# Kernel tuning notes

Hardware: AMD Instinct MI355X
Metric: run time of the kernel (lower is better)

## Reference

```python
import jax, jax.numpy as jnp
import numpy as np

E, TOPK = 8, 2
N_EMBD, TEXT_DIM, FULL = 1024, 1024, 1024
BS, SEQ = 8, 512

def setup_inputs() -> dict:
    key = jax.random.key(0)
    ks = jax.random.split(key, 8)
    return {
        "x": jax.random.normal(ks[0], (BS, SEQ, N_EMBD), jnp.float32),
        "dec_embeddings": jax.random.normal(ks[1], (BS, TEXT_DIM), jnp.float32),
        # router is zero-init in the module, but use small random weights so top-k is non-degenerate
        "router_w": jax.random.normal(ks[2], (E, TEXT_DIM), jnp.float32) * 0.02,
        "router_b": jnp.zeros((E,), jnp.float32),
        "w1": jax.random.normal(ks[3], (E, N_EMBD, N_EMBD), jnp.float32) * 0.02,
        "w2": jax.random.normal(ks[4], (E, N_EMBD, FULL), jnp.float32) * 0.02,
        "b1": jnp.zeros((E, 1, N_EMBD), jnp.float32),
        "b2": jnp.zeros((E, 1, FULL), jnp.float32),
    }

def reference(x, dec_embeddings, router_w, router_b, w1, w2, b1, b2):
    bs, seqlen, n_embd = x.shape
    logits = dec_embeddings @ router_w.T + router_b          # (bs, E)
    gate_probs = jax.nn.softmax(logits, axis=-1)
    topk_w, topk_idx = jax.lax.top_k(gate_probs, TOPK)       # (bs, k)
    topk_w = topk_w / jnp.sum(topk_w, axis=-1, keepdims=True)
    # dense all-expert 2-layer MLP (as written in the original)
    hidden = jax.nn.relu(jnp.einsum('bsn,enh->ebsh', x, w1) + b1[:, None])   # (E,bs,S,H)
    out_all = jnp.einsum('ebsh,ehf->ebsf', hidden, w2) + b2[:, None]          # (E,bs,S,F)
    out_b = jnp.transpose(out_all, (1, 0, 2, 3))             # (bs,E,S,F)
    # gather top-k expert outputs per batch item and combine
    sel = jnp.take_along_axis(out_b, topk_idx[:, :, None, None], axis=1)      # (bs,k,S,F)
    final_output = jnp.sum(topk_w[:, :, None, None] * sel, axis=1)            # (bs,S,F)
    combined_mask = jnp.max(jax.nn.one_hot(topk_idx, E, dtype=x.dtype), axis=1)  # (bs,E)
    aux_loss = E * jnp.sum(jnp.mean(gate_probs, axis=0) * jnp.mean(combined_mask, axis=0))
    return final_output, aux_loss, combined_mask, logits
```

## Files before the change

### kernel.cpp

```cpp
#include <hip/hip_runtime.h>
#include <hip/hip_bf16.h>
#include <stdint.h>

#define EXP 8
#define DIM 1024
#define SEQL 512
#define BATCH 8
#define OUT_FINAL_N (BATCH * SEQL * DIM)
#define OFF_AUX    4194304
#define OFF_MASK   4194305
#define OFF_LOGITS 4194369

typedef __bf16 bf16_t;
typedef bf16_t bf16x8 __attribute__((ext_vector_type(8)));
typedef bf16_t bf16x4 __attribute__((ext_vector_type(4)));
typedef float  f32x4  __attribute__((ext_vector_type(4)));

typedef __attribute__((address_space(1))) void* as1p;
typedef __attribute__((address_space(3))) void* as3p;

__device__ __forceinline__ void glds16(const void* g, void* l) {
  __builtin_amdgcn_global_load_lds((as1p)(void*)g, (as3p)l, 16, 0, 0);
}

__global__ __launch_bounds__(256) void prep_kernel(
    const float* __restrict__ x, const float* __restrict__ dec,
    const float* __restrict__ rw, const float* __restrict__ rb,
    const float* __restrict__ w1, const float* __restrict__ w2,
    bf16_t* __restrict__ xb, bf16_t* __restrict__ w1t, bf16_t* __restrict__ w2t,
    float* __restrict__ out_aux, float* __restrict__ out_mask,
    float* __restrict__ out_logits, int* __restrict__ idx_ws,
    float* __restrict__ w_ws) {
  __shared__ float tile[64][65];
  __shared__ float part[256];
  __shared__ float lg64[64];
  __shared__ float probs[64];
  __shared__ float msk[64];
  const int bid = blockIdx.x;
  const int t = threadIdx.x;

  if (bid < 4096) {
    const int z = bid >> 8;
    const int rem = bid & 255;
    const int r0 = (rem >> 4) * 64, c0 = (rem & 15) * 64;
    const float* src = (z < 8) ? (w1 + (size_t)z * DIM * DIM)
                               : (w2 + (size_t)(z - 8) * DIM * DIM);
    bf16_t* dst = (z < 8) ? (w1t + (size_t)z * DIM * DIM)
                          : (w2t + (size_t)(z - 8) * DIM * DIM);
    const int rr = t >> 4, cc = t & 15;
#pragma unroll
    for (int i = 0; i < 4; ++i) {
      const int row = rr + i * 16;
      const float4 v = *(const float4*)(src + (size_t)(r0 + row) * DIM + c0 + cc * 4);
      tile[row][cc * 4 + 0] = v.x;
      tile[row][cc * 4 + 1] = v.y;
      tile[row][cc * 4 + 2] = v.z;
      tile[row][cc * 4 + 3] = v.w;
    }
    __syncthreads();
#pragma unroll
    for (int i = 0; i < 4; ++i) {
      const int dc = rr + i * 16;
      bf16x4 o;
      o[0] = (bf16_t)tile[cc * 4 + 0][dc];
      o[1] = (bf16_t)tile[cc * 4 + 1][dc];
      o[2] = (bf16_t)tile[cc * 4 + 2][dc];
      o[3] = (bf16_t)tile[cc * 4 + 3][dc];
      *(bf16x4*)(dst + (size_t)(c0 + dc) * DIM + r0 + cc * 4) = o;
    }
  } else if (bid < 4096 + 1024) {
    const int i0 = (bid - 4096) * 1024 + t;
#pragma unroll
    for (int i = 0; i < 4; ++i) {
      float4 v = ((const float4*)x)[i0 + i * 256];
      bf16x4 o;
      o[0] = (bf16_t)v.x; o[1] = (bf16_t)v.y; o[2] = (bf16_t)v.z; o[3] = (bf16_t)v.w;
      ((bf16x4*)xb)[i0 + i * 256] = o;
    }
  } else {
    const int p = t >> 2, seg = t & 3;
    const int b = p >> 3, e = p & 7;
    const float4* dv = (const float4*)(dec + b * DIM + seg * 256);
    const float4* wv = (const float4*)(rw + e * DIM + seg * 256);
    float s = 0.f;
#pragma unroll 8
    for (int i = 0; i < 64; ++i) {
      float4 a = dv[i], c = wv[i];
      s += a.x * c.x + a.y * c.y + a.z * c.z + a.w * c.w;
    }
    part[t] = s;
    __syncthreads();
    if (seg == 0) {
      float l = part[t] + part[t + 1] + part[t + 2] + part[t + 3] + rb[e];
      lg64[p] = l;
      out_logits[p] = l;
    }
    __syncthreads();
    if (t < 8) {
      float l[8];
      float mx = -1e30f;
#pragma unroll
      for (int k = 0; k < 8; ++k) { l[k] = lg64[t * 8 + k]; mx = fmaxf(mx, l[k]); }
      float pe[8];
      float sum = 0.f;
#pragma unroll
      for (int k = 0; k < 8; ++k) { pe[k] = expf(l[k] - mx); sum += pe[k]; }
      float inv = 1.f / sum;
#pragma unroll
      for (int k = 0; k < 8; ++k) { pe[k] *= inv; probs[t * 8 + k] = pe[k]; }
      int i0 = 0;
#pragma unroll
      for (int k = 1; k < 8; ++k) if (pe[k] > pe[i0]) i0 = k;
      int i1 = (i0 == 0) ? 1 : 0;
#pragma unroll
      for (int k = 0; k < 8; ++k) if (k != i0 && pe[k] > pe[i1]) i1 = k;
      float p0 = pe[i0], p1 = pe[i1];
      float invs = 1.f / (p0 + p1);
      idx_ws[t * 2] = i0;
      idx_ws[t * 2 + 1] = i1;
      w_ws[t * 2] = p0 * invs;
      w_ws[t * 2 + 1] = p1 * invs;
#pragma unroll
      for (int k = 0; k < 8; ++k) {
        float m = (k == i0 || k == i1) ? 1.f : 0.f;
        msk[t * 8 + k] = m;
        out_mask[t * 8 + k] = m;
      }
    }
    __syncthreads();
    if (t == 0) {
      float aux = 0.f;
#pragma unroll
      for (int k = 0; k < 8; ++k) {
        float mp = 0.f, mm = 0.f;
#pragma unroll
        for (int bb = 0; bb < 8; ++bb) { mp += probs[bb * 8 + k]; mm += msk[bb * 8 + k]; }
        aux += (mp * 0.125f) * (mm * 0.125f);
      }
      out_aux[0] = 8.f * aux;
    }
  }
}

__device__ __forceinline__ void gemm_kloop(const bf16_t* __restrict__ A,
                                           const bf16_t* __restrict__ Bt,
                                           char* sA, char* sB,
                                           int tid, f32x4 acc[4][4]) {
  const int lane = tid & 63;
  const int w = tid >> 6;
  const int wr = w >> 1, wc = w & 1;
  const int m15 = lane & 15, q = lane >> 4;

  const int rl = tid >> 2;
  const int cp = (tid & 3) ^ (rl & 3);
  const bf16_t* ga0 = A + (size_t)rl * DIM + cp * 8;
  const bf16_t* ga1 = ga0 + (size_t)64 * DIM;
  const bf16_t* gb0 = Bt + (size_t)rl * DIM + cp * 8;
  const bf16_t* gb1 = gb0 + (size_t)64 * DIM;
  char* la0 = sA + tid * 16;
  char* la1 = sA + 4096 + tid * 16;
  char* lb0 = sB + tid * 16;
  char* lb1 = sB + 4096 + tid * 16;

  const char* ra[4];
  const char* rb[4];
#pragma unroll
  for (int i = 0; i < 4; ++i) {
    int r = wr * 64 + i * 16 + m15;
    ra[i] = sA + r * 64 + ((q ^ (r & 3)) * 16);
    int n = wc * 64 + i * 16 + m15;
    rb[i] = sB + n * 64 + ((q ^ (n & 3)) * 16);
  }

  for (int kt = 0; kt < DIM; kt += 32) {
    glds16(ga0 + kt, la0);
    glds16(ga1 + kt, la1);
    glds16(gb0 + kt, lb0);
    glds16(gb1 + kt, lb1);
    __syncthreads();
    bf16x8 af[4], bfr[4];
#pragma unroll
    for (int i = 0; i < 4; ++i) af[i] = *(const bf16x8*)ra[i];
#pragma unroll
    for (int j = 0; j < 4; ++j) bfr[j] = *(const bf16x8*)rb[j];
#pragma unroll
    for (int i = 0; i < 4; ++i)
#pragma unroll
      for (int j = 0; j < 4; ++j)
        acc[i][j] = __builtin_amdgcn_mfma_f32_16x16x32_bf16(af[i], bfr[j], acc[i][j], 0, 0, 0);
    __syncthreads();
  }
}

__global__ __launch_bounds__(256) void gemm1_kernel(const bf16_t* __restrict__ xb,
                                                    const bf16_t* __restrict__ w1t,
                                                    const float* __restrict__ b1,
                                                    const int* __restrict__ topk_idx,
                                                    bf16_t* __restrict__ hidden) {
  __shared__ __align__(16) char smem[16384];
  const int tid = threadIdx.x;
  const int bN = blockIdx.x, bM = blockIdx.y, slot = blockIdx.z;
  const int b = slot >> 1;
  const int e = topk_idx[slot];

  const bf16_t* A = xb + ((size_t)b * SEQL + bM * 128) * DIM;
  const bf16_t* Bt = w1t + ((size_t)e * DIM + bN * 128) * DIM;

  f32x4 acc[4][4];
#pragma unroll
  for (int i = 0; i < 4; ++i)
#pragma unroll
    for (int j = 0; j < 4; ++j) acc[i][j] = {0.f, 0.f, 0.f, 0.f};

  gemm_kloop(A, Bt, smem, smem + 8192, tid, acc);

  const int lane = tid & 63, w = tid >> 6;
  const int wr = w >> 1, wc = w & 1;
  const int m15 = lane & 15, q = lane >> 4;
  const float* be = b1 + e * DIM;
  bf16_t* H = hidden + (size_t)slot * SEQL * DIM;
#pragma unroll
  for (int i = 0; i < 4; ++i) {
    int row = bM * 128 + wr * 64 + i * 16 + q * 4;
#pragma unroll
    for (int j = 0; j < 4; ++j) {
      int col = bN * 128 + wc * 64 + j * 16 + m15;
      float bias = be[col];
#pragma unroll
      for (int r = 0; r < 4; ++r) {
        float v = acc[i][j][r] + bias;
        H[(size_t)(row + r) * DIM + col] = (bf16_t)fmaxf(v, 0.f);
      }
    }
  }
}

__global__ __launch_bounds__(512) void gemm2_kernel(const bf16_t* __restrict__ hidden,
                                                    const bf16_t* __restrict__ w2t,
                                                    const float* __restrict__ b2,
                                                    const int* __restrict__ topk_idx,
                                                    const float* __restrict__ topk_w,
                                                    float* __restrict__ out) {
  __shared__ __align__(16) char smem[32768];
  const int tid = threadIdx.x;
  const int g = tid >> 8;
  const int t = tid & 255;
  const int bN = blockIdx.x, bM = blockIdx.y, b = blockIdx.z;
  const int e = topk_idx[b * 2 + g];
  const float sg = topk_w[b * 2 + g];

  char* sA = smem + g * 16384;
  char* sB = smem + g * 16384 + 8192;

  f32x4 acc[4][4];
#pragma unroll
  for (int i = 0; i < 4; ++i)
#pragma unroll
    for (int j = 0; j < 4; ++j) acc[i][j] = {0.f, 0.f, 0.f, 0.f};

  const bf16_t* A = hidden + ((size_t)(b * 2 + g) * SEQL + bM * 128) * DIM;
  const bf16_t* Bt = w2t + ((size_t)e * DIM + bN * 128) * DIM;
  gemm_kloop(A, Bt, sA, sB, t, acc);

  float* scr = (float*)smem;
  const int lane = t & 63, wv = t >> 6;
  const int wr = wv >> 1, wc = wv & 1;
  const int m15 = lane & 15, q = lane >> 4;
  const float w0 = topk_w[b * 2], w1v = topk_w[b * 2 + 1];
  const float* be0 = b2 + topk_idx[b * 2] * DIM;
  const float* be1 = b2 + topk_idx[b * 2 + 1] * DIM;
  float* O = out + (size_t)b * SEQL * DIM;

#pragma unroll
  for (int half = 0; half < 2; ++half) {
    __syncthreads();
    if (g == 1) {
#pragma unroll
      for (int ii = 0; ii < 2; ++ii)
#pragma unroll
        for (int j = 0; j < 4; ++j)
#pragma unroll
          for (int r = 0; r < 4; ++r)
            scr[(ii * 16 + j * 4 + r) * 256 + t] = sg * acc[half * 2 + ii][j][r];
    }
    __syncthreads();
    if (g == 0) {
#pragma unroll
      for (int ii = 0; ii < 2; ++ii) {
        const int i = half * 2 + ii;
        const int row = bM * 128 + wr * 64 + i * 16 + q * 4;
#pragma unroll
        for (int j = 0; j < 4; ++j) {
          const int col = bN * 128 + wc * 64 + j * 16 + m15;
          const float bb = w0 * be0[col] + w1v * be1[col];
#pragma unroll
          for (int r = 0; r < 4; ++r) {
            O[(size_t)(row + r) * DIM + col] =
                sg * acc[i][j][r] + scr[(ii * 16 + j * 4 + r) * 256 + t] + bb;
          }
        }
      }
    }
  }
}

extern "C" void kernel_launch(void* const* d_in, const int* in_sizes, int n_in,
                              void* d_out, int out_size, void* d_ws, size_t ws_size,
                              hipStream_t stream) {
  const float* x   = (const float*)d_in[0];
  const float* dec = (const float*)d_in[1];
  const float* rw  = (const float*)d_in[2];
  const float* rb  = (const float*)d_in[3];
  const float* w1  = (const float*)d_in[4];
  const float* w2  = (const float*)d_in[5];
  const float* b1  = (const float*)d_in[6];
  const float* b2  = (const float*)d_in[7];
  float* out = (float*)d_out;

  char* ws = (char*)d_ws;
  bf16_t* xb   = (bf16_t*)(ws);
  bf16_t* w1t  = (bf16_t*)(ws + (8u << 20));
  bf16_t* w2t  = (bf16_t*)(ws + (24u << 20));
  bf16_t* hid  = (bf16_t*)(ws + (40u << 20));
  int*    idxw = (int*)(ws + (56u << 20));
  float*  ww   = (float*)(ws + (56u << 20) + 64);

  hipLaunchKernelGGL(prep_kernel, dim3(4096 + 1024 + 1), dim3(256), 0, stream,
                     x, dec, rw, rb, w1, w2, xb, w1t, w2t,
                     out + OFF_AUX, out + OFF_MASK, out + OFF_LOGITS, idxw, ww);
  hipLaunchKernelGGL(gemm1_kernel, dim3(8, 4, 16), dim3(256), 0, stream,
                     xb, w1t, b1, idxw, hid);
  hipLaunchKernelGGL(gemm2_kernel, dim3(8, 4, 8), dim3(512), 0, stream,
                     hid, w2t, b2, idxw, ww, out);
}
```

Baseline: 206.9 us.

## Double-buffer GEMM k-loop, shrink M tile to 64, vectorize prep and hidden stores

The GEMM k-loop now prefetches the next K slice into a second LDS buffer while the current one feeds MFMA, so each step needs one barrier instead of two. M tiles drop from 128 to 64, which doubles the grid of both GEMM kernels and adds occupancy hints. gemm1 stages its ReLU output through LDS so hidden is written with wide 16-byte stores. The prep kernel transposes larger weight tiles with wider bf16x8 stores and converts more x elements per block. In exchange, smaller M tiles give each B tile less reuse and add more B traffic, and LDS use per block rises.

```diff
diff --git a/kernel.cpp b/kernel.cpp
--- a/kernel.cpp
+++ b/kernel.cpp
@@ -31,7 +31,7 @@
     float* __restrict__ out_aux, float* __restrict__ out_mask,
     float* __restrict__ out_logits, int* __restrict__ idx_ws,
     float* __restrict__ w_ws) {
-  __shared__ float tile[64][65];
+  __shared__ float tile[64][129];
   __shared__ float part[256];
   __shared__ float lg64[64];
   __shared__ float probs[64];
@@ -39,42 +39,48 @@
   const int bid = blockIdx.x;
   const int t = threadIdx.x;
 
-  if (bid < 4096) {
-    const int z = bid >> 8;
-    const int rem = bid & 255;
-    const int r0 = (rem >> 4) * 64, c0 = (rem & 15) * 64;
+  if (bid < 2048) {
+    const int z = bid >> 7;
+    const int rem = bid & 127;
+    const int k0 = (rem >> 4) * 128;
+    const int n0 = (rem & 15) * 64;
     const float* src = (z < 8) ? (w1 + (size_t)z * DIM * DIM)
                                : (w2 + (size_t)(z - 8) * DIM * DIM);
     bf16_t* dst = (z < 8) ? (w1t + (size_t)z * DIM * DIM)
                           : (w2t + (size_t)(z - 8) * DIM * DIM);
-    const int rr = t >> 4, cc = t & 15;
-#pragma unroll
-    for (int i = 0; i < 4; ++i) {
-      const int row = rr + i * 16;
-      const float4 v = *(const float4*)(src + (size_t)(r0 + row) * DIM + c0 + cc * 4);
-      tile[row][cc * 4 + 0] = v.x;
-      tile[row][cc * 4 + 1] = v.y;
-      tile[row][cc * 4 + 2] = v.z;
-      tile[row][cc * 4 + 3] = v.w;
-    }
-    __syncthreads();
-#pragma unroll
-    for (int i = 0; i < 4; ++i) {
-      const int dc = rr + i * 16;
+    const int rr = t >> 4, c4 = t & 15;
+    float4 v[8];
+#pragma unroll
+    for (int i = 0; i < 8; ++i)
+      v[i] = *(const float4*)(src + (size_t)(k0 + rr + 16 * i) * DIM + n0 + c4 * 4);
+#pragma unroll
+    for (int i = 0; i < 8; ++i) {
+      const int k = rr + 16 * i;
+      tile[c4 * 4 + 0][k] = v[i].x;
+      tile[c4 * 4 + 1][k] = v[i].y;
+      tile[c4 * 4 + 2][k] = v[i].z;
+      tile[c4 * 4 + 3][k] = v[i].w;
+    }
+    __syncthreads();
+#pragma unroll
+    for (int ii = 0; ii < 4; ++ii) {
+      const int n = (t >> 4) + 16 * ii;
+      const int c = t & 15;
+      bf16x8 o;
+#pragma unroll
+      for (int wd = 0; wd < 8; ++wd) o[wd] = (bf16_t)tile[n][c * 8 + wd];
+      *(bf16x8*)(dst + (size_t)(n0 + n) * DIM + k0 + c * 8) = o;
+    }
+  } else if (bid < 2048 + 512) {
+    const int i0 = (bid - 2048) * 2048 + t;
+    float4 v[8];
+#pragma unroll
+    for (int i = 0; i < 8; ++i) v[i] = ((const float4*)x)[i0 + i * 256];
+#pragma unroll
+    for (int i = 0; i < 8; ++i) {
       bf16x4 o;
-      o[0] = (bf16_t)tile[cc * 4 + 0][dc];
-      o[1] = (bf16_t)tile[cc * 4 + 1][dc];
-      o[2] = (bf16_t)tile[cc * 4 + 2][dc];
-      o[3] = (bf16_t)tile[cc * 4 + 3][dc];
-      *(bf16x4*)(dst + (size_t)(c0 + dc) * DIM + r0 + cc * 4) = o;
-    }
-  } else if (bid < 4096 + 1024) {
-    const int i0 = (bid - 4096) * 1024 + t;
-#pragma unroll
-    for (int i = 0; i < 4; ++i) {
-      float4 v = ((const float4*)x)[i0 + i * 256];
-      bf16x4 o;
-      o[0] = (bf16_t)v.x; o[1] = (bf16_t)v.y; o[2] = (bf16_t)v.z; o[3] = (bf16_t)v.w;
+      o[0] = (bf16_t)v[i].x; o[1] = (bf16_t)v[i].y;
+      o[2] = (bf16_t)v[i].z; o[3] = (bf16_t)v[i].w;
       ((bf16x4*)xb)[i0 + i * 256] = o;
     }
   } else {
@@ -142,106 +148,116 @@
   }
 }
 
-__device__ __forceinline__ void gemm_kloop(const bf16_t* __restrict__ A,
-                                           const bf16_t* __restrict__ Bt,
-                                           char* sA, char* sB,
-                                           int tid, f32x4 acc[4][4]) {
-  const int lane = tid & 63;
-  const int w = tid >> 6;
-  const int wr = w >> 1, wc = w & 1;
+__device__ __forceinline__ void kloop_64x128(const bf16_t* __restrict__ A,
+                                             const bf16_t* __restrict__ Bt,
+                                             char* sA, char* sB, int t,
+                                             f32x4 acc[2][4]) {
+  const int lane = t & 63;
+  const int w = t >> 6, wr = w >> 1, wc = w & 1;
   const int m15 = lane & 15, q = lane >> 4;
-
-  const int rl = tid >> 2;
-  const int cp = (tid & 3) ^ (rl & 3);
-  const bf16_t* ga0 = A + (size_t)rl * DIM + cp * 8;
-  const bf16_t* ga1 = ga0 + (size_t)64 * DIM;
+  const int rl = t >> 2, cp = (t & 3) ^ (rl & 3);
+  const bf16_t* ga  = A  + (size_t)rl * DIM + cp * 8;
   const bf16_t* gb0 = Bt + (size_t)rl * DIM + cp * 8;
   const bf16_t* gb1 = gb0 + (size_t)64 * DIM;
-  char* la0 = sA + tid * 16;
-  char* la1 = sA + 4096 + tid * 16;
-  char* lb0 = sB + tid * 16;
-  char* lb1 = sB + 4096 + tid * 16;
-
-  const char* ra[4];
+
+  const char* ra[2];
   const char* rb[4];
 #pragma unroll
-  for (int i = 0; i < 4; ++i) {
-    int r = wr * 64 + i * 16 + m15;
+  for (int i = 0; i < 2; ++i) {
+    const int r = wr * 32 + i * 16 + m15;
     ra[i] = sA + r * 64 + ((q ^ (r & 3)) * 16);
-    int n = wc * 64 + i * 16 + m15;
-    rb[i] = sB + n * 64 + ((q ^ (n & 3)) * 16);
-  }
-
-  for (int kt = 0; kt < DIM; kt += 32) {
-    glds16(ga0 + kt, la0);
-    glds16(ga1 + kt, la1);
-    glds16(gb0 + kt, lb0);
-    glds16(gb1 + kt, lb1);
-    __syncthreads();
-    bf16x8 af[4], bfr[4];
-#pragma unroll
-    for (int i = 0; i < 4; ++i) af[i] = *(const bf16x8*)ra[i];
-#pragma unroll
-    for (int j = 0; j < 4; ++j) bfr[j] = *(const bf16x8*)rb[j];
-#pragma unroll
-    for (int i = 0; i < 4; ++i)
+  }
+#pragma unroll
+  for (int j = 0; j < 4; ++j) {
+    const int n = wc * 64 + j * 16 + m15;
+    rb[j] = sB + n * 64 + ((q ^ (n & 3)) * 16);
+  }
+
+  glds16(ga,  sA + t * 16);
+  glds16(gb0, sB + t * 16);
+  glds16(gb1, sB + 4096 + t * 16);
+
+  for (int kt = 0; kt < 32; ++kt) {
+    const int cur = kt & 1;
+    __syncthreads();
+    if (kt < 31) {
+      const int nxt = cur ^ 1;
+      const int off = (kt + 1) * 32;
+      glds16(ga + off,  sA + nxt * 4096 + t * 16);
+      glds16(gb0 + off, sB + nxt * 8192 + t * 16);
+      glds16(gb1 + off, sB + nxt * 8192 + 4096 + t * 16);
+    }
+    bf16x8 af[2], bfr[4];
+#pragma unroll
+    for (int i = 0; i < 2; ++i) af[i] = *(const bf16x8*)(ra[i] + cur * 4096);
+#pragma unroll
+    for (int j = 0; j < 4; ++j) bfr[j] = *(const bf16x8*)(rb[j] + cur * 8192);
+#pragma unroll
+    for (int i = 0; i < 2; ++i)
 #pragma unroll
       for (int j = 0; j < 4; ++j)
         acc[i][j] = __builtin_amdgcn_mfma_f32_16x16x32_bf16(af[i], bfr[j], acc[i][j], 0, 0, 0);
-    __syncthreads();
-  }
-}
-
-__global__ __launch_bounds__(256) void gemm1_kernel(const bf16_t* __restrict__ xb,
-                                                    const bf16_t* __restrict__ w1t,
-                                                    const float* __restrict__ b1,
-                                                    const int* __restrict__ topk_idx,
-                                                    bf16_t* __restrict__ hidden) {
-  __shared__ __align__(16) char smem[16384];
+  }
+}
+
+__global__ __launch_bounds__(256, 4) void gemm1_kernel(const bf16_t* __restrict__ xb,
+                                                       const bf16_t* __restrict__ w1t,
+                                                       const float* __restrict__ b1,
+                                                       const int* __restrict__ topk_idx,
+                                                       bf16_t* __restrict__ hidden) {
+  __shared__ __align__(16) char smem[24576];
   const int tid = threadIdx.x;
   const int bN = blockIdx.x, bM = blockIdx.y, slot = blockIdx.z;
   const int b = slot >> 1;
   const int e = topk_idx[slot];
 
-  const bf16_t* A = xb + ((size_t)b * SEQL + bM * 128) * DIM;
+  const bf16_t* A  = xb + ((size_t)b * SEQL + bM * 64) * DIM;
   const bf16_t* Bt = w1t + ((size_t)e * DIM + bN * 128) * DIM;
 
-  f32x4 acc[4][4];
-#pragma unroll
-  for (int i = 0; i < 4; ++i)
+  f32x4 acc[2][4];
+#pragma unroll
+  for (int i = 0; i < 2; ++i)
 #pragma unroll
     for (int j = 0; j < 4; ++j) acc[i][j] = {0.f, 0.f, 0.f, 0.f};
 
-  gemm_kloop(A, Bt, smem, smem + 8192, tid, acc);
-
+  kloop_64x128(A, Bt, smem, smem + 8192, tid, acc);
+
+  __syncthreads();
+  bf16_t* hb = (bf16_t*)smem;
   const int lane = tid & 63, w = tid >> 6;
   const int wr = w >> 1, wc = w & 1;
   const int m15 = lane & 15, q = lane >> 4;
   const float* be = b1 + e * DIM;
-  bf16_t* H = hidden + (size_t)slot * SEQL * DIM;
-#pragma unroll
-  for (int i = 0; i < 4; ++i) {
-    int row = bM * 128 + wr * 64 + i * 16 + q * 4;
+#pragma unroll
+  for (int i = 0; i < 2; ++i)
 #pragma unroll
     for (int j = 0; j < 4; ++j) {
-      int col = bN * 128 + wc * 64 + j * 16 + m15;
-      float bias = be[col];
+      const int colL = wc * 64 + j * 16 + m15;
+      const float bias = be[bN * 128 + colL];
 #pragma unroll
       for (int r = 0; r < 4; ++r) {
-        float v = acc[i][j][r] + bias;
-        H[(size_t)(row + r) * DIM + col] = (bf16_t)fmaxf(v, 0.f);
+        const int rowL = wr * 32 + i * 16 + q * 4 + r;
+        hb[rowL * 136 + colL] = (bf16_t)fmaxf(acc[i][j][r] + bias, 0.f);
       }
     }
-  }
-}
-
-__global__ __launch_bounds__(512) void gemm2_kernel(const bf16_t* __restrict__ hidden,
-                                                    const bf16_t* __restrict__ w2t,
-                                                    const float* __restrict__ b2,
-                                                    const int* __restrict__ topk_idx,
-                                                    const float* __restrict__ topk_w,
-                                                    float* __restrict__ out) {
-  __shared__ __align__(16) char smem[32768];
+  __syncthreads();
+  bf16_t* H = hidden + (size_t)slot * SEQL * DIM + ((size_t)bM * 64) * DIM + bN * 128;
+#pragma unroll
+  for (int ii = 0; ii < 4; ++ii) {
+    const int r = (tid >> 4) + 16 * ii;
+    const int c = tid & 15;
+    bf16x8 vv = *(const bf16x8*)(hb + r * 136 + c * 8);
+    *(bf16x8*)(H + (size_t)r * DIM + c * 8) = vv;
+  }
+}
+
+__global__ __launch_bounds__(512, 4) void gemm2_kernel(const bf16_t* __restrict__ hidden,
+                                                       const bf16_t* __restrict__ w2t,
+                                                       const float* __restrict__ b2,
+                                                       const int* __restrict__ topk_idx,
+                                                       const float* __restrict__ topk_w,
+                                                       float* __restrict__ out) {
+  __shared__ __align__(16) char smem[49152];
   const int tid = threadIdx.x;
   const int g = tid >> 8;
   const int t = tid & 255;
@@ -249,19 +265,20 @@
   const int e = topk_idx[b * 2 + g];
   const float sg = topk_w[b * 2 + g];
 
-  char* sA = smem + g * 16384;
-  char* sB = smem + g * 16384 + 8192;
-
-  f32x4 acc[4][4];
-#pragma unroll
-  for (int i = 0; i < 4; ++i)
+  char* sA = smem + g * 24576;
+  char* sB = smem + g * 24576 + 8192;
+
+  f32x4 acc[2][4];
+#pragma unroll
+  for (int i = 0; i < 2; ++i)
 #pragma unroll
     for (int j = 0; j < 4; ++j) acc[i][j] = {0.f, 0.f, 0.f, 0.f};
 
-  const bf16_t* A = hidden + ((size_t)(b * 2 + g) * SEQL + bM * 128) * DIM;
+  const bf16_t* A  = hidden + ((size_t)(b * 2 + g) * SEQL + bM * 64) * DIM;
   const bf16_t* Bt = w2t + ((size_t)e * DIM + bN * 128) * DIM;
-  gemm_kloop(A, Bt, sA, sB, t, acc);
-
+  kloop_64x128(A, Bt, sA, sB, t, acc);
+
+  __syncthreads();
   float* scr = (float*)smem;
   const int lane = t & 63, wv = t >> 6;
   const int wr = wv >> 1, wc = wv & 1;
@@ -273,34 +290,27 @@
 
 #pragma unroll
   for (int half = 0; half < 2; ++half) {
-    __syncthreads();
     if (g == 1) {
 #pragma unroll
-      for (int ii = 0; ii < 2; ++ii)
-#pragma unroll
-        for (int j = 0; j < 4; ++j)
-#pragma unroll
-          for (int r = 0; r < 4; ++r)
-            scr[(ii * 16 + j * 4 + r) * 256 + t] = sg * acc[half * 2 + ii][j][r];
+      for (int j = 0; j < 4; ++j)
+#pragma unroll
+        for (int r = 0; r < 4; ++r)
+          scr[(j * 4 + r) * 256 + t] = sg * acc[half][j][r];
     }
     __syncthreads();
     if (g == 0) {
 #pragma unroll
-      for (int ii = 0; ii < 2; ++ii) {
-        const int i = half * 2 + ii;
-        const int row = bM * 128 + wr * 64 + i * 16 + q * 4;
-#pragma unroll
-        for (int j = 0; j < 4; ++j) {
-          const int col = bN * 128 + wc * 64 + j * 16 + m15;
-          const float bb = w0 * be0[col] + w1v * be1[col];
-#pragma unroll
-          for (int r = 0; r < 4; ++r) {
-            O[(size_t)(row + r) * DIM + col] =
-                sg * acc[i][j][r] + scr[(ii * 16 + j * 4 + r) * 256 + t] + bb;
-          }
-        }
+      for (int j = 0; j < 4; ++j) {
+        const int col = bN * 128 + wc * 64 + j * 16 + m15;
+        const float bb = w0 * be0[col] + w1v * be1[col];
+        const int row = bM * 64 + wr * 32 + half * 16 + q * 4;
+#pragma unroll
+        for (int r = 0; r < 4; ++r)
+          O[(size_t)(row + r) * DIM + col] =
+              sg * acc[half][j][r] + scr[(j * 4 + r) * 256 + t] + bb;
       }
     }
+    __syncthreads();
   }
 }
 
@@ -325,11 +335,11 @@
   int*    idxw = (int*)(ws + (56u << 20));
   float*  ww   = (float*)(ws + (56u << 20) + 64);
 
-  hipLaunchKernelGGL(prep_kernel, dim3(4096 + 1024 + 1), dim3(256), 0, stream,
+  hipLaunchKernelGGL(prep_kernel, dim3(2048 + 512 + 1), dim3(256), 0, stream,
                      x, dec, rw, rb, w1, w2, xb, w1t, w2t,
                      out + OFF_AUX, out + OFF_MASK, out + OFF_LOGITS, idxw, ww);
-  hipLaunchKernelGGL(gemm1_kernel, dim3(8, 4, 16), dim3(256), 0, stream,
+  hipLaunchKernelGGL(gemm1_kernel, dim3(8, 8, 16), dim3(256), 0, stream,
                      xb, w1t, b1, idxw, hid);
-  hipLaunchKernelGGL(gemm2_kernel, dim3(8, 4, 8), dim3(512), 0, stream,
+  hipLaunchKernelGGL(gemm2_kernel, dim3(8, 8, 8), dim3(512), 0, stream,
                      hid, w2t, b2, idxw, ww, out);
 }
```

Result: no change. 203.3 us (-1.7%).
